# Performance work log

Hardware: AMD Instinct MI355X
Metric: run time of the kernel (lower is better)

The kernel has to match this reference:

```python
import jax, jax.numpy as jnp
import numpy as np

EPS = 1e-5

def _layernorm(x, g, b):
    mu = jnp.mean(x, axis=-1, keepdims=True)
    var = jnp.mean(jnp.square(x - mu), axis=-1, keepdims=True)
    return (x - mu) * jax.lax.rsqrt(var + EPS) * g + b

def setup_inputs() -> dict:
    key = jax.random.key(0)
    ks = jax.random.split(key, 5)
    F_, H, D = 1024, 16, 64
    B, N = 4, 2048
    s = lambda k, shp, fan: jax.random.normal(k, shp, jnp.float32) * (fan ** -0.5)
    return {
        "x": jax.random.normal(ks[0], (B, N, F_), jnp.float32),
        "Wq": s(ks[1], (H * D, F_), F_),
        "Wkv": s(ks[2], (2 * H * D, F_), F_),
        "Wo": s(ks[3], (F_, H * D), H * D),
        "ln_g": jnp.ones((F_,), jnp.float32),
        "ln_b": jnp.zeros((F_,), jnp.float32),
        "lnc_g": jnp.ones((F_,), jnp.float32),
        "lnc_b": jnp.zeros((F_,), jnp.float32),
    }

def reference(x, Wq, Wkv, Wo, ln_g, ln_b, lnc_g, lnc_b):
    H, D = 16, 64
    scale = D ** -0.5
    skip = x
    xn = _layernorm(x, ln_g, ln_b)          # query path norm
    cn = _layernorm(x, lnc_g, lnc_b)        # context (self) norm
    B, N, _ = x.shape
    q = jnp.einsum('bnf,ef->bne', xn, Wq)   # [B,N,H*D]
    kv = jnp.einsum('bnf,ef->bne', cn, Wkv) # [B,N,2*H*D]
    k, v = jnp.split(kv, 2, axis=-1)
    tohd = lambda t: t.reshape(B, N, H, D).transpose(0, 2, 1, 3)  # b h n d
    q, k, v = tohd(q), tohd(k), tohd(v)
    sim = jnp.einsum('bhnd,bhmd->bhnm', q, k) * scale
    attn = jax.nn.softmax(sim, axis=-1)
    out = jnp.einsum('bhnm,bhmd->bhnd', attn, v)
    out = out.transpose(0, 2, 1, 3).reshape(B, N, H * D)
    out = jnp.einsum('bne,fe->bnf', out, Wo)
    return skip + out
```

## Files before the change

### kernel.cpp

```cpp
#include <hip/hip_runtime.h>
#include <hip/hip_bf16.h>
#include <stdint.h>

typedef __bf16 bf16;
typedef __bf16 bf16x8 __attribute__((ext_vector_type(8)));
typedef __bf16 bf16x4 __attribute__((ext_vector_type(4)));
typedef float f32x4 __attribute__((ext_vector_type(4)));
typedef unsigned u32x2 __attribute__((ext_vector_type(2)));

#define F_DIM 1024
#define NSEQ  2048
#define NB    4
#define NH    16
#define HD    64
#define MROWS (NB * NSEQ)

__device__ __forceinline__ void gload_lds16(const void* g, void* l) {
    __builtin_amdgcn_global_load_lds(
        (__attribute__((address_space(1))) void*)g,
        (__attribute__((address_space(3))) void*)l,
        16, 0, 0);
}

__device__ __forceinline__ unsigned lds_addr(const void* p) {
    return (unsigned)(size_t)(__attribute__((address_space(3))) const void*)p;
}

__global__ __launch_bounds__(256) void ln2_kernel(
    const float* __restrict__ x,
    const float* __restrict__ g1, const float* __restrict__ b1,
    const float* __restrict__ g2, const float* __restrict__ b2,
    bf16* __restrict__ xn, bf16* __restrict__ cn)
{
    const int row = blockIdx.x;
    const int t = threadIdx.x;
    float4 v = reinterpret_cast<const float4*>(x + (size_t)row * F_DIM)[t];
    float s  = v.x + v.y + v.z + v.w;
    float ss = v.x * v.x + v.y * v.y + v.z * v.z + v.w * v.w;
#pragma unroll
    for (int m = 1; m < 64; m <<= 1) {
        s  += __shfl_xor(s, m);
        ss += __shfl_xor(ss, m);
    }
    __shared__ float red[8];
    const int w = t >> 6;
    if ((t & 63) == 0) { red[w] = s; red[4 + w] = ss; }
    __syncthreads();
    s  = red[0] + red[1] + red[2] + red[3];
    ss = red[4] + red[5] + red[6] + red[7];
    const float mu  = s * (1.0f / F_DIM);
    const float var = fmaxf(ss * (1.0f / F_DIM) - mu * mu, 0.0f);
    const float rs  = rsqrtf(var + 1e-5f);

    float4 G1 = reinterpret_cast<const float4*>(g1)[t];
    float4 B1 = reinterpret_cast<const float4*>(b1)[t];
    float4 G2 = reinterpret_cast<const float4*>(g2)[t];
    float4 B2 = reinterpret_cast<const float4*>(b2)[t];
    const float h0 = (v.x - mu) * rs, h1 = (v.y - mu) * rs;
    const float h2 = (v.z - mu) * rs, h3 = (v.w - mu) * rs;
    bf16x4 o1 = { (bf16)(h0 * G1.x + B1.x), (bf16)(h1 * G1.y + B1.y),
                  (bf16)(h2 * G1.z + B1.z), (bf16)(h3 * G1.w + B1.w) };
    bf16x4 o2 = { (bf16)(h0 * G2.x + B2.x), (bf16)(h1 * G2.y + B2.y),
                  (bf16)(h2 * G2.z + B2.z), (bf16)(h3 * G2.w + B2.w) };
    *reinterpret_cast<bf16x4*>(xn + (size_t)row * F_DIM + t * 4) = o1;
    *reinterpret_cast<bf16x4*>(cn + (size_t)row * F_DIM + t * 4) = o2;
}

__global__ __launch_bounds__(256) void cvt_kernel(
    const float* __restrict__ src, bf16* __restrict__ dst, int n4)
{
    int i = blockIdx.x * 256 + threadIdx.x;
    if (i < n4) {
        float4 v = reinterpret_cast<const float4*>(src)[i];
        bf16x4 o = { (bf16)v.x, (bf16)v.y, (bf16)v.z, (bf16)v.w };
        reinterpret_cast<bf16x4*>(dst)[i] = o;
    }
}

template <int EPI>
__global__ __launch_bounds__(256, 2) void gemm_bt(
    const bf16* __restrict__ A, const bf16* __restrict__ B,
    bf16* __restrict__ Cb, float* __restrict__ Cf,
    const float* __restrict__ skip, int M, int N, int K, float oscale)
{
    __shared__ bf16 As[128 * 32];
    __shared__ bf16 Bs[128 * 32];
    const int t = threadIdx.x;
    const int lane = t & 63;
    const int w = t >> 6;
    const int wr = w >> 1, wc = w & 1;
    const int bm = blockIdx.y * 128;
    const int bn = blockIdx.x * 128;
    const int r = lane & 15;
    const int kg = (lane >> 4) * 8;

    f32x4 acc[4][4];
#pragma unroll
    for (int i = 0; i < 4; i++)
#pragma unroll
        for (int j = 0; j < 4; j++) acc[i][j] = (f32x4){0.f, 0.f, 0.f, 0.f};

    const int c0 = t, c1 = 256 + t;
    const size_t aoff0 = (size_t)(bm + (c0 >> 2)) * K + (c0 & 3) * 8;
    const size_t aoff1 = (size_t)(bm + (c1 >> 2)) * K + (c1 & 3) * 8;
    const size_t boff0 = (size_t)(bn + (c0 >> 2)) * K + (c0 & 3) * 8;
    const size_t boff1 = (size_t)(bn + (c1 >> 2)) * K + (c1 & 3) * 8;
    bf16* lA0 = As + (size_t)(0 * 256 + w * 64) * 8;
    bf16* lA1 = As + (size_t)(1 * 256 + w * 64) * 8;
    bf16* lB0 = Bs + (size_t)(0 * 256 + w * 64) * 8;
    bf16* lB1 = Bs + (size_t)(1 * 256 + w * 64) * 8;

    for (int kt = 0; kt < K; kt += 32) {
        gload_lds16(A + aoff0 + kt, lA0);
        gload_lds16(A + aoff1 + kt, lA1);
        gload_lds16(B + boff0 + kt, lB0);
        gload_lds16(B + boff1 + kt, lB1);
        __syncthreads();
        bf16x8 af[4], bfr[4];
#pragma unroll
        for (int mi = 0; mi < 4; mi++)
            af[mi] = *(const bf16x8*)(As + (wr * 64 + mi * 16 + r) * 32 + kg);
#pragma unroll
        for (int ni = 0; ni < 4; ni++)
            bfr[ni] = *(const bf16x8*)(Bs + (wc * 64 + ni * 16 + r) * 32 + kg);
#pragma unroll
        for (int mi = 0; mi < 4; mi++)
#pragma unroll
            for (int ni = 0; ni < 4; ni++)
                acc[mi][ni] = __builtin_amdgcn_mfma_f32_16x16x32_bf16(
                    af[mi], bfr[ni], acc[mi][ni], 0, 0, 0);
        __syncthreads();
    }

    const int g = lane >> 4;
#pragma unroll
    for (int mi = 0; mi < 4; mi++) {
#pragma unroll
        for (int ni = 0; ni < 4; ni++) {
            const int col = bn + wc * 64 + ni * 16 + r;
#pragma unroll
            for (int j = 0; j < 4; j++) {
                const int row = bm + wr * 64 + mi * 16 + g * 4 + j;
                const float vv = acc[mi][ni][j];
                if (EPI == 0) {
                    Cb[(size_t)row * N + col] = (bf16)(vv * oscale);
                } else {
                    Cf[(size_t)row * N + col] = vv + skip[(size_t)row * N + col];
                }
            }
        }
    }
}

__global__ __launch_bounds__(256, 4) void attn_kernel(
    const bf16* __restrict__ q, const bf16* __restrict__ kvp,
    bf16* __restrict__ o)
{
    __shared__ __align__(16) bf16 Ks[64 * 64];
    __shared__ __align__(16) bf16 Vs[64 * 64];
    __shared__ __align__(16) bf16 Ps[4][16 * 72];

    const int bid = blockIdx.x;
    const int idx = (bid & 7) * 256 + (bid >> 3);
    const int bh = idx >> 5;
    const int qt = idx & 31;
    const int b = bh >> 4, h = bh & 15;

    const int t = threadIdx.x, lane = t & 63, w = t >> 6;
    const int r = lane & 15, g = lane >> 4;

    const size_t rowq = (size_t)b * NSEQ;

    size_t ksrc[2], vsrc[2];
#pragma unroll
    for (int c = 0; c < 2; c++) {
        const int p = c * 256 + t;
        const int krow = p >> 3;
        const int kcol = (p & 7) ^ (krow & 7);
        ksrc[c] = (size_t)(rowq + krow) * (2 * F_DIM) + h * HD + kcol * 8;
        const int kvb = p >> 5, dblk = (p >> 3) & 3;
        const int kvl = (p & 7) >> 1, d8 = p & 1;
        vsrc[c] = (size_t)(rowq + kvb * 4 + kvl) * (2 * F_DIM) + F_DIM + h * HD
                  + dblk * 16 + d8 * 8;
    }
    bf16* kdst0 = Ks + (0 * 256 + (t & ~63)) * 8;
    bf16* kdst1 = Ks + (1 * 256 + (t & ~63)) * 8;
    bf16* vdst0 = Vs + (0 * 256 + (t & ~63)) * 8;
    bf16* vdst1 = Vs + (1 * 256 + (t & ~63)) * 8;

    const int q0 = qt * 64 + w * 16;
    bf16x8 qf[2];
#pragma unroll
    for (int kk = 0; kk < 2; kk++)
        qf[kk] = *(const bf16x8*)(q + (rowq + q0 + r) * F_DIM + h * HD + kk * 32 + g * 8);

    f32x4 oacc[4];
#pragma unroll
    for (int i = 0; i < 4; i++) oacc[i] = (f32x4){0.f, 0.f, 0.f, 0.f};
    float m_r = -1e30f, l_r = 0.f;

    const unsigned va = lds_addr(Vs) + (unsigned)(g * 1024 + r * 8);

    for (int kv0 = 0; kv0 < NSEQ; kv0 += 64) {
        const size_t koff = (size_t)kv0 * (2 * F_DIM);
        __syncthreads();
        gload_lds16(kvp + ksrc[0] + koff, kdst0);
        gload_lds16(kvp + ksrc[1] + koff, kdst1);
        gload_lds16(kvp + vsrc[0] + koff, vdst0);
        gload_lds16(kvp + vsrc[1] + koff, vdst1);
        __syncthreads();

        f32x4 s4[4];
#pragma unroll
        for (int nt = 0; nt < 4; nt++) s4[nt] = (f32x4){0.f, 0.f, 0.f, 0.f};
#pragma unroll
        for (int kk = 0; kk < 2; kk++) {
#pragma unroll
            for (int nt = 0; nt < 4; nt++) {
                const unsigned lb = (unsigned)((nt * 16 + r) * 128 + kk * 64 + g * 16)
                                    ^ (unsigned)((r & 7) << 4);
                bf16x8 kf = *(const bf16x8*)((const char*)Ks + lb);
                s4[nt] = __builtin_amdgcn_mfma_f32_16x16x32_bf16(kf, qf[kk], s4[nt], 0, 0, 0);
            }
        }

        float mx = s4[0][0];
#pragma unroll
        for (int nt = 0; nt < 4; nt++)
#pragma unroll
            for (int j = 0; j < 4; j++) mx = fmaxf(mx, s4[nt][j]);
        mx = fmaxf(mx, __shfl_xor(mx, 16));
        mx = fmaxf(mx, __shfl_xor(mx, 32));
        const float mnew = fmaxf(m_r, mx);
        const float alpha = __expf(m_r - mnew);
        float ps = 0.f;
#pragma unroll
        for (int nt = 0; nt < 4; nt++)
#pragma unroll
            for (int j = 0; j < 4; j++) {
                const float pp = __expf(s4[nt][j] - mnew);
                s4[nt][j] = pp;
                ps += pp;
            }
        ps += __shfl_xor(ps, 16);
        ps += __shfl_xor(ps, 32);
        l_r = l_r * alpha + ps;
        m_r = mnew;

#pragma unroll
        for (int nt = 0; nt < 4; nt++) {
            bf16x4 pb = { (bf16)s4[nt][0], (bf16)s4[nt][1],
                          (bf16)s4[nt][2], (bf16)s4[nt][3] };
            *(bf16x4*)&Ps[w][r * 72 + nt * 16 + g * 4] = pb;
        }

#pragma unroll
        for (int j = 0; j < 4; j++) {
            const float aj = __shfl(alpha, g * 4 + j);
#pragma unroll
            for (int ntd = 0; ntd < 4; ntd++) oacc[ntd][j] *= aj;
        }

        bf16x8 pf[2];
#pragma unroll
        for (int kk = 0; kk < 2; kk++)
            pf[kk] = *(const bf16x8*)&Ps[w][r * 72 + kk * 32 + g * 8];

        u32x2 vt[4][2][2];
#pragma unroll
        for (int ntd = 0; ntd < 4; ntd++)
#pragma unroll
            for (int kk = 0; kk < 2; kk++) {
                const unsigned a = va + (unsigned)(kk * 4096 + ntd * 128);
                asm volatile("ds_read_b64_tr_b16 %0, %2\n\t"
                             "ds_read_b64_tr_b16 %1, %2 offset:512"
                             : "=&v"(vt[ntd][kk][0]), "=&v"(vt[ntd][kk][1])
                             : "v"(a));
            }
        asm volatile("s_waitcnt lgkmcnt(0)" ::: "memory");
        __builtin_amdgcn_sched_barrier(0);

#pragma unroll
        for (int ntd = 0; ntd < 4; ntd++)
#pragma unroll
            for (int kk = 0; kk < 2; kk++) {
                union { u32x2 h[2]; bf16x8 v; } u;
                u.h[0] = vt[ntd][kk][0];
                u.h[1] = vt[ntd][kk][1];
                oacc[ntd] = __builtin_amdgcn_mfma_f32_16x16x32_bf16(pf[kk], u.v, oacc[ntd], 0, 0, 0);
            }
    }

    float rl[4];
#pragma unroll
    for (int j = 0; j < 4; j++) {
        const float lj = __shfl(l_r, g * 4 + j);
        rl[j] = 1.0f / lj;
    }
#pragma unroll
    for (int ntd = 0; ntd < 4; ntd++)
#pragma unroll
        for (int j = 0; j < 4; j++) {
            const int row = q0 + g * 4 + j;
            o[(rowq + row) * F_DIM + h * HD + ntd * 16 + r] =
                (bf16)(oacc[ntd][j] * rl[j]);
        }
}

extern "C" void kernel_launch(void* const* d_in, const int* in_sizes, int n_in,
                              void* d_out, int out_size, void* d_ws, size_t ws_size,
                              hipStream_t stream)
{
    const float* x     = (const float*)d_in[0];
    const float* Wq    = (const float*)d_in[1];
    const float* Wkv   = (const float*)d_in[2];
    const float* Wo    = (const float*)d_in[3];
    const float* ln_g  = (const float*)d_in[4];
    const float* ln_b  = (const float*)d_in[5];
    const float* lnc_g = (const float*)d_in[6];
    const float* lnc_b = (const float*)d_in[7];
    float* out = (float*)d_out;

    bf16* xn   = (bf16*)d_ws;
    bf16* cn   = xn  + (size_t)MROWS * F_DIM;
    bf16* qb   = cn  + (size_t)MROWS * F_DIM;
    bf16* kvb  = qb  + (size_t)MROWS * F_DIM;
    bf16* wqb  = kvb + (size_t)MROWS * 2 * F_DIM;
    bf16* wkvb = wqb + (size_t)F_DIM * F_DIM;
    bf16* wob  = wkvb + (size_t)2 * F_DIM * F_DIM;
    bf16* ao   = xn;

    ln2_kernel<<<dim3(MROWS), dim3(256), 0, stream>>>(x, ln_g, ln_b, lnc_g, lnc_b, xn, cn);

    cvt_kernel<<<dim3((F_DIM * F_DIM / 4 + 255) / 256), dim3(256), 0, stream>>>(Wq, wqb, F_DIM * F_DIM / 4);
    cvt_kernel<<<dim3((2 * F_DIM * F_DIM / 4 + 255) / 256), dim3(256), 0, stream>>>(Wkv, wkvb, 2 * F_DIM * F_DIM / 4);
    cvt_kernel<<<dim3((F_DIM * F_DIM / 4 + 255) / 256), dim3(256), 0, stream>>>(Wo, wob, F_DIM * F_DIM / 4);

    gemm_bt<0><<<dim3(F_DIM / 128, MROWS / 128), dim3(256), 0, stream>>>(
        xn, wqb, qb, nullptr, nullptr, MROWS, F_DIM, F_DIM, 0.125f);
    gemm_bt<0><<<dim3(2 * F_DIM / 128, MROWS / 128), dim3(256), 0, stream>>>(
        cn, wkvb, kvb, nullptr, nullptr, MROWS, 2 * F_DIM, F_DIM, 1.0f);
    attn_kernel<<<dim3(NSEQ / 64 * NB * NH), dim3(256), 0, stream>>>(qb, kvb, ao);
    gemm_bt<1><<<dim3(F_DIM / 128, MROWS / 128), dim3(256), 0, stream>>>(
        ao, wob, nullptr, out, x, MROWS, F_DIM, F_DIM, 1.0f);
}
```

Measured before the change: 258.9 us.

## Double-buffer attention KV loads, exp2 softmax with lazy rescale, XCD-swizzle GEMM tiles

The attention kernel now double-buffers K/V tiles in LDS and prefetches the next tile while computing the current one. This removes one barrier per iteration and hides global-load latency. Softmax uses exp2 with log2(e) folded into the Q projection scale. It skips the running-max rescale of the accumulators unless the max grows by more than 8, which cuts ALU and shuffle work. Other changes: s_setprio raises priority around the MFMA blocks, and GEMM block indices are remapped so neighbouring tiles share an XCD for L2 reuse. The costs are twice the LDS, which may reduce occupancy, and bf16 rounding of the rounded-up exponentials when rescaling is deferred.

```diff
diff --git a/kernel.cpp b/kernel.cpp
--- a/kernel.cpp
+++ b/kernel.cpp
@@ -14,6 +14,7 @@
 #define NH    16
 #define HD    64
 #define MROWS (NB * NSEQ)
+#define LOG2E 1.44269504088896340736f
 
 __device__ __forceinline__ void gload_lds16(const void* g, void* l) {
     __builtin_amdgcn_global_load_lds(
@@ -89,8 +90,14 @@
     const int lane = t & 63;
     const int w = t >> 6;
     const int wr = w >> 1, wc = w & 1;
-    const int bm = blockIdx.y * 128;
-    const int bn = blockIdx.x * 128;
+
+    int flat = blockIdx.y * gridDim.x + blockIdx.x;
+    const int nwg = gridDim.x * gridDim.y;
+    if ((nwg & 7) == 0)
+        flat = (flat & 7) * (nwg >> 3) + (flat >> 3);
+    const int bm = (flat / gridDim.x) * 128;
+    const int bn = (flat % gridDim.x) * 128;
+
     const int r = lane & 15;
     const int kg = (lane >> 4) * 8;
 
@@ -156,8 +163,8 @@
     const bf16* __restrict__ q, const bf16* __restrict__ kvp,
     bf16* __restrict__ o)
 {
-    __shared__ __align__(16) bf16 Ks[64 * 64];
-    __shared__ __align__(16) bf16 Vs[64 * 64];
+    __shared__ __align__(16) bf16 Ks[2][64 * 64];
+    __shared__ __align__(16) bf16 Vs[2][64 * 64];
     __shared__ __align__(16) bf16 Ps[4][16 * 72];
 
     const int bid = blockIdx.x;
@@ -183,10 +190,6 @@
         vsrc[c] = (size_t)(rowq + kvb * 4 + kvl) * (2 * F_DIM) + F_DIM + h * HD
                   + dblk * 16 + d8 * 8;
     }
-    bf16* kdst0 = Ks + (0 * 256 + (t & ~63)) * 8;
-    bf16* kdst1 = Ks + (1 * 256 + (t & ~63)) * 8;
-    bf16* vdst0 = Vs + (0 * 256 + (t & ~63)) * 8;
-    bf16* vdst1 = Vs + (1 * 256 + (t & ~63)) * 8;
 
     const int q0 = qt * 64 + w * 16;
     bf16x8 qf[2];
@@ -199,53 +202,79 @@
     for (int i = 0; i < 4; i++) oacc[i] = (f32x4){0.f, 0.f, 0.f, 0.f};
     float m_r = -1e30f, l_r = 0.f;
 
-    const unsigned va = lds_addr(Vs) + (unsigned)(g * 1024 + r * 8);
-
-    for (int kv0 = 0; kv0 < NSEQ; kv0 += 64) {
-        const size_t koff = (size_t)kv0 * (2 * F_DIM);
-        __syncthreads();
-        gload_lds16(kvp + ksrc[0] + koff, kdst0);
-        gload_lds16(kvp + ksrc[1] + koff, kdst1);
-        gload_lds16(kvp + vsrc[0] + koff, vdst0);
-        gload_lds16(kvp + vsrc[1] + koff, vdst1);
-        __syncthreads();
+    const unsigned va = lds_addr(Vs[0]) + (unsigned)(g * 1024 + r * 8);
+    const unsigned wbase = (unsigned)(t & ~63) * 8;
+
+    {
+        bf16* kb = Ks[0] + wbase;
+        bf16* vb = Vs[0] + wbase;
+        gload_lds16(kvp + ksrc[0], kb);
+        gload_lds16(kvp + ksrc[1], kb + 2048);
+        gload_lds16(kvp + vsrc[0], vb);
+        gload_lds16(kvp + vsrc[1], vb + 2048);
+    }
+
+    int cur = 0;
+    for (int kv0 = 0; kv0 < NSEQ; kv0 += 64, cur ^= 1) {
+        asm volatile("s_waitcnt vmcnt(0)" ::: "memory");
+        __builtin_amdgcn_s_barrier();
+
+        if (kv0 + 64 < NSEQ) {
+            const size_t koff = (size_t)(kv0 + 64) * (2 * F_DIM);
+            bf16* kb = Ks[cur ^ 1] + wbase;
+            bf16* vb = Vs[cur ^ 1] + wbase;
+            gload_lds16(kvp + ksrc[0] + koff, kb);
+            gload_lds16(kvp + ksrc[1] + koff, kb + 2048);
+            gload_lds16(kvp + vsrc[0] + koff, vb);
+            gload_lds16(kvp + vsrc[1] + koff, vb + 2048);
+        }
 
         f32x4 s4[4];
 #pragma unroll
         for (int nt = 0; nt < 4; nt++) s4[nt] = (f32x4){0.f, 0.f, 0.f, 0.f};
+        __builtin_amdgcn_s_setprio(1);
 #pragma unroll
         for (int kk = 0; kk < 2; kk++) {
 #pragma unroll
             for (int nt = 0; nt < 4; nt++) {
                 const unsigned lb = (unsigned)((nt * 16 + r) * 128 + kk * 64 + g * 16)
                                     ^ (unsigned)((r & 7) << 4);
-                bf16x8 kf = *(const bf16x8*)((const char*)Ks + lb);
+                bf16x8 kf = *(const bf16x8*)((const char*)Ks[cur] + lb);
                 s4[nt] = __builtin_amdgcn_mfma_f32_16x16x32_bf16(kf, qf[kk], s4[nt], 0, 0, 0);
             }
         }
-
-        float mx = s4[0][0];
-#pragma unroll
-        for (int nt = 0; nt < 4; nt++)
-#pragma unroll
-            for (int j = 0; j < 4; j++) mx = fmaxf(mx, s4[nt][j]);
+        __builtin_amdgcn_s_setprio(0);
+
+        float mx = fmaxf(fmaxf(fmaxf(s4[0][0], s4[0][1]), fmaxf(s4[0][2], s4[0][3])),
+                         fmaxf(fmaxf(s4[1][0], s4[1][1]), fmaxf(s4[1][2], s4[1][3])));
+        mx = fmaxf(mx, fmaxf(fmaxf(fmaxf(s4[2][0], s4[2][1]), fmaxf(s4[2][2], s4[2][3])),
+                             fmaxf(fmaxf(s4[3][0], s4[3][1]), fmaxf(s4[3][2], s4[3][3]))));
         mx = fmaxf(mx, __shfl_xor(mx, 16));
         mx = fmaxf(mx, __shfl_xor(mx, 32));
-        const float mnew = fmaxf(m_r, mx);
-        const float alpha = __expf(m_r - mnew);
+        if (!__all(mx <= m_r + 8.0f)) {
+            const float mnew = fmaxf(m_r, mx);
+            const float alpha = exp2f(m_r - mnew);
+            l_r *= alpha;
+#pragma unroll
+            for (int j = 0; j < 4; j++) {
+                const float aj = __shfl(alpha, g * 4 + j);
+#pragma unroll
+                for (int ntd = 0; ntd < 4; ntd++) oacc[ntd][j] *= aj;
+            }
+            m_r = mnew;
+        }
         float ps = 0.f;
 #pragma unroll
         for (int nt = 0; nt < 4; nt++)
 #pragma unroll
             for (int j = 0; j < 4; j++) {
-                const float pp = __expf(s4[nt][j] - mnew);
+                const float pp = exp2f(s4[nt][j] - m_r);
                 s4[nt][j] = pp;
                 ps += pp;
             }
         ps += __shfl_xor(ps, 16);
         ps += __shfl_xor(ps, 32);
-        l_r = l_r * alpha + ps;
-        m_r = mnew;
+        l_r += ps;
 
 #pragma unroll
         for (int nt = 0; nt < 4; nt++) {
@@ -254,24 +283,18 @@
             *(bf16x4*)&Ps[w][r * 72 + nt * 16 + g * 4] = pb;
         }
 
-#pragma unroll
-        for (int j = 0; j < 4; j++) {
-            const float aj = __shfl(alpha, g * 4 + j);
-#pragma unroll
-            for (int ntd = 0; ntd < 4; ntd++) oacc[ntd][j] *= aj;
-        }
-
         bf16x8 pf[2];
 #pragma unroll
         for (int kk = 0; kk < 2; kk++)
             pf[kk] = *(const bf16x8*)&Ps[w][r * 72 + kk * 32 + g * 8];
 
         u32x2 vt[4][2][2];
+        const unsigned vab = va + (unsigned)(cur * 8192);
 #pragma unroll
         for (int ntd = 0; ntd < 4; ntd++)
 #pragma unroll
             for (int kk = 0; kk < 2; kk++) {
-                const unsigned a = va + (unsigned)(kk * 4096 + ntd * 128);
+                const unsigned a = vab + (unsigned)(kk * 4096 + ntd * 128);
                 asm volatile("ds_read_b64_tr_b16 %0, %2\n\t"
                              "ds_read_b64_tr_b16 %1, %2 offset:512"
                              : "=&v"(vt[ntd][kk][0]), "=&v"(vt[ntd][kk][1])
@@ -280,6 +303,7 @@
         asm volatile("s_waitcnt lgkmcnt(0)" ::: "memory");
         __builtin_amdgcn_sched_barrier(0);
 
+        __builtin_amdgcn_s_setprio(1);
 #pragma unroll
         for (int ntd = 0; ntd < 4; ntd++)
 #pragma unroll
@@ -289,6 +313,7 @@
                 u.h[1] = vt[ntd][kk][1];
                 oacc[ntd] = __builtin_amdgcn_mfma_f32_16x16x32_bf16(pf[kk], u.v, oacc[ntd], 0, 0, 0);
             }
+        __builtin_amdgcn_s_setprio(0);
     }
 
     float rl[4];
@@ -337,7 +362,7 @@
     cvt_kernel<<<dim3((F_DIM * F_DIM / 4 + 255) / 256), dim3(256), 0, stream>>>(Wo, wob, F_DIM * F_DIM / 4);
 
     gemm_bt<0><<<dim3(F_DIM / 128, MROWS / 128), dim3(256), 0, stream>>>(
-        xn, wqb, qb, nullptr, nullptr, MROWS, F_DIM, F_DIM, 0.125f);
+        xn, wqb, qb, nullptr, nullptr, MROWS, F_DIM, F_DIM, 0.125f * LOG2E);
     gemm_bt<0><<<dim3(2 * F_DIM / 128, MROWS / 128), dim3(256), 0, stream>>>(
         cn, wkvb, kvb, nullptr, nullptr, MROWS, 2 * F_DIM, F_DIM, 1.0f);
     attn_kernel<<<dim3(NSEQ / 64 * NB * NH), dim3(256), 0, stream>>>(qb, kvb, ao);
```

Result: slower. 288.1 us (+11.3%).
